# Kernel tuning notes

Measured on AMD Instinct MI355X. Metric: run time of the kernel, lower is better.

The kernel has to match this reference:

```python
import jax, jax.numpy as jnp
import numpy as np
import math

H = 1024
N = 64
DT_MIN, DT_MAX = 1e-3, 1e-1
L_SEQ = 4096


def setup_inputs() -> dict:
    key = jax.random.key(0)
    k1, k2, k3 = jax.random.split(key, 3)
    # C ~ complex normal, stored as (..., 2) real view like torch.view_as_real
    C = jax.random.normal(k1, (H, N // 2, 2), dtype=jnp.float32)
    # log_dt ~ U[log(dt_min), log(dt_max)]
    log_dt = jax.random.uniform(k2, (H,), dtype=jnp.float32) * (
        math.log(DT_MAX) - math.log(DT_MIN)
    ) + math.log(DT_MIN)
    # log_A_real = log(0.5), A_imag = pi * arange(N/2) repeated over H
    log_A_real = jnp.full((H, N // 2), math.log(0.5), dtype=jnp.float32)
    A_imag = math.pi * jnp.broadcast_to(
        jnp.arange(N // 2, dtype=jnp.float32), (H, N // 2)
    )
    return {"C": C, "log_dt": log_dt, "log_A_real": log_A_real, "A_imag": A_imag, "L": L_SEQ}


def reference(C, log_dt, log_A_real, A_imag, L):
    dt = jnp.exp(log_dt)                                  # (H,)
    Cc = jax.lax.complex(C[..., 0], C[..., 1])            # (H, N/2) complex
    A = -jnp.exp(log_A_real) + 1j * A_imag                # (H, N/2) complex
    dtA = A * dt[:, None]                                 # (H, N/2)
    # Vandermonde: exp(dtA * l) for l in [0, L)
    K = dtA[:, :, None] * jnp.arange(L, dtype=jnp.float32)  # (H, N/2, L)
    Cm = Cc * (jnp.exp(dtA) - 1.0) / A                    # (H, N/2)
    K = 2.0 * jnp.einsum("hn,hnl->hl", Cm, jnp.exp(K)).real  # (H, L)
    return K
```

## Files before the change

kernel.cpp:

```cpp
#include <hip/hip_runtime.h>
#include <hip/hip_bf16.h>
#include <math.h>


#define H_DIM 1024
#define NH 32
#define L_DIM 4096
#define TPB 256
#define PER 16
#define STRIDE_F 72

__global__ __launch_bounds__(TPB) void s4d_kernel(
    const float* __restrict__ C,
    const float* __restrict__ log_dt,
    const float* __restrict__ log_A_real,
    const float* __restrict__ A_imag,
    float* __restrict__ out)
{
    const int h = blockIdx.x;
    const int t = threadIdx.x;

    __shared__ float lds[NH * STRIDE_F];

    const double INV_2PI = 0.15915494309189533576888376337251;

    {
        const int n = t & 31;
        const int s = t >> 5;
        const float dtf = __expf(log_dt[h]);
        const float arf = -__expf(log_A_real[h * NH + n]);
        const float aif = A_imag[h * NH + n];
        const float are = arf * dtf;
        const double th_rev = (double)aif * (double)dtf * INV_2PI;

        float* base = &lds[n * STRIDE_F];

#pragma unroll
        for (int e = 0; e < 2; ++e) {
            const int j = 2 * s + e;
            {
                const int l = 16 * j;
                const float mag = __expf(are * (float)l);
                double u = (double)l * th_rev;
                u -= floor(u);
                const float uf = (float)u;
                base[8 + 2 * j]     = mag * __builtin_amdgcn_cosf(uf);
                base[8 + 2 * j + 1] = mag * __builtin_amdgcn_sinf(uf);
            }
            {
                const int l = 256 * j;
                const float mag = __expf(are * (float)l);
                double u = (double)l * th_rev;
                u -= floor(u);
                const float uf = (float)u;
                base[40 + 2 * j]     = mag * __builtin_amdgcn_cosf(uf);
                base[40 + 2 * j + 1] = mag * __builtin_amdgcn_sinf(uf);
            }
        }

        if (s == 0) {
            const float mag = __expf(are);
            double u = th_rev - floor(th_rev);
            const float uf = (float)u;
            const float wr = mag * __builtin_amdgcn_cosf(uf);
            const float wi = mag * __builtin_amdgcn_sinf(uf);
            const float cr = C[(h * NH + n) * 2 + 0];
            const float ci = C[(h * NH + n) * 2 + 1];
            const float er = wr - 1.0f;
            const float ei = wi;
            const float tr = cr * er - ci * ei;
            const float ti = cr * ei + ci * er;
            const float inv = 2.0f / (arf * arf + aif * aif);
            base[0] = wr;
            base[1] = wi;
            base[2] = (tr * arf + ti * aif) * inv;
            base[3] = (ti * arf - tr * aif) * inv;
            base[4] = wr + wr;
            base[5] = -(wr * wr + wi * wi);
        }
    }
    __syncthreads();

    float acc[PER];
#pragma unroll
    for (int j = 0; j < PER; ++j) acc[j] = 0.0f;

    const int ta_i = t & 15;
    const int tb_i = t >> 4;

#pragma unroll 2
    for (int n = 0; n < NH; ++n) {
        const float* base = &lds[n * STRIDE_F];
        const float4 hdr = *(const float4*)base;
        const float2 pq  = *(const float2*)(base + 4);
        const float2 ta  = *(const float2*)(base + 8 + 2 * ta_i);
        const float2 tb  = *(const float2*)(base + 40 + 2 * tb_i);

        const float pr = ta.x * tb.x - ta.y * tb.y;
        const float pi = ta.x * tb.y + ta.y * tb.x;
        const float zr = hdr.z * pr - hdr.w * pi;
        const float zi = hdr.z * pi + hdr.w * pr;

        float x0 = zr;
        float x1 = zr * hdr.x - zi * hdr.y;
        acc[0] += x0;
        acc[1] += x1;
        float tq = pq.y * x0;
#pragma unroll
        for (int j = 2; j < PER; ++j) {
            const float x2 = fmaf(pq.x, x1, tq);
            tq = pq.y * x1;
            acc[j] += x2;
            x0 = x1;
            x1 = x2;
        }
    }

    float4* op = (float4*)(out + (size_t)h * L_DIM + (size_t)t * PER);
#pragma unroll
    for (int j = 0; j < PER / 4; ++j) {
        op[j] = make_float4(acc[4 * j], acc[4 * j + 1], acc[4 * j + 2], acc[4 * j + 3]);
    }
}

extern "C" void kernel_launch(void* const* d_in, const int* in_sizes, int n_in,
                              void* d_out, int out_size, void* d_ws, size_t ws_size,
                              hipStream_t stream) {
    const float* C          = (const float*)d_in[0];
    const float* log_dt     = (const float*)d_in[1];
    const float* log_A_real = (const float*)d_in[2];
    const float* A_imag     = (const float*)d_in[3];
    float* out = (float*)d_out;

    s4d_kernel<<<dim3(H_DIM), dim3(TPB), 0, stream>>>(C, log_dt, log_A_real, A_imag, out);
}
```

Before: 79.16 us.

## Split sequence across two blocks per head and fold Cm into base table

Launches two blocks per head, each covering half of L, so each thread now runs an 8-step recurrence instead of 16. The fine-grained table (32 entries at stride 8) is premultiplied by Cm and the block offset, which removes a complex multiply from the inner loop. The launch bounds now request higher occupancy. The cost is that the per-block table setup (transcendentals in double-precision range reduction) runs twice as often across the grid, and the shorter recurrence gives a different accuracy profile.

```diff
diff --git a/kernel.cpp b/kernel.cpp
--- a/kernel.cpp
+++ b/kernel.cpp
@@ -6,19 +6,24 @@
 #define H_DIM 1024
 #define NH 32
 #define L_DIM 4096
+#define SPLIT 2
+#define L_BLK (L_DIM / SPLIT)
 #define TPB 256
-#define PER 16
-#define STRIDE_F 72
+#define PER 8
+#define NTA 32
+#define NTB 8
+#define STRIDE_F 84
 
-__global__ __launch_bounds__(TPB) void s4d_kernel(
+__global__ __launch_bounds__(TPB, 8) void s4d_kernel(
     const float* __restrict__ C,
     const float* __restrict__ log_dt,
     const float* __restrict__ log_A_real,
     const float* __restrict__ A_imag,
     float* __restrict__ out)
 {
-    const int h = blockIdx.x;
-    const int t = threadIdx.x;
+    const int h   = blockIdx.x;
+    const int off = blockIdx.y * L_BLK;
+    const int t   = threadIdx.x;
 
     __shared__ float lds[NH * STRIDE_F];
 
@@ -27,56 +32,57 @@
     {
         const int n = t & 31;
         const int s = t >> 5;
+
         const float dtf = __expf(log_dt[h]);
         const float arf = -__expf(log_A_real[h * NH + n]);
         const float aif = A_imag[h * NH + n];
         const float are = arf * dtf;
         const double th_rev = (double)aif * (double)dtf * INV_2PI;
 
+        const float mw = __expf(are);
+        const float u1 = (float)(th_rev - floor(th_rev));
+        const float wr = mw * __builtin_amdgcn_cosf(u1);
+        const float wi = mw * __builtin_amdgcn_sinf(u1);
+
+        const float cr = C[(h * NH + n) * 2 + 0];
+        const float ci = C[(h * NH + n) * 2 + 1];
+        const float er = wr - 1.0f;
+        const float ei = wi;
+        const float tr = cr * er - ci * ei;
+        const float ti = cr * ei + ci * er;
+        const float inv = 2.0f / (arf * arf + aif * aif);
+        const float cmr = (tr * arf + ti * aif) * inv;
+        const float cmi = (ti * arf - tr * aif) * inv;
+
         float* base = &lds[n * STRIDE_F];
 
 #pragma unroll
-        for (int e = 0; e < 2; ++e) {
-            const int j = 2 * s + e;
-            {
-                const int l = 16 * j;
-                const float mag = __expf(are * (float)l);
-                double u = (double)l * th_rev;
-                u -= floor(u);
-                const float uf = (float)u;
-                base[8 + 2 * j]     = mag * __builtin_amdgcn_cosf(uf);
-                base[8 + 2 * j + 1] = mag * __builtin_amdgcn_sinf(uf);
-            }
-            {
-                const int l = 256 * j;
-                const float mag = __expf(are * (float)l);
-                double u = (double)l * th_rev;
-                u -= floor(u);
-                const float uf = (float)u;
-                base[40 + 2 * j]     = mag * __builtin_amdgcn_cosf(uf);
-                base[40 + 2 * j + 1] = mag * __builtin_amdgcn_sinf(uf);
-            }
+        for (int k = 0; k < 4; ++k) {
+            const int i = s + 8 * k;
+            const int l = off + 8 * i;
+            const float mag = __expf(are * (float)l);
+            double u = (double)l * th_rev;
+            u -= floor(u);
+            const float uf = (float)u;
+            const float br = mag * __builtin_amdgcn_cosf(uf);
+            const float bi = mag * __builtin_amdgcn_sinf(uf);
+            base[4 + 2 * i]     = cmr * br - cmi * bi;
+            base[4 + 2 * i + 1] = cmr * bi + cmi * br;
         }
-
+        {
+            const int l = 256 * s;
+            const float mag = __expf(are * (float)l);
+            double u = (double)l * th_rev;
+            u -= floor(u);
+            const float uf = (float)u;
+            base[68 + 2 * s]     = mag * __builtin_amdgcn_cosf(uf);
+            base[68 + 2 * s + 1] = mag * __builtin_amdgcn_sinf(uf);
+        }
         if (s == 0) {
-            const float mag = __expf(are);
-            double u = th_rev - floor(th_rev);
-            const float uf = (float)u;
-            const float wr = mag * __builtin_amdgcn_cosf(uf);
-            const float wi = mag * __builtin_amdgcn_sinf(uf);
-            const float cr = C[(h * NH + n) * 2 + 0];
-            const float ci = C[(h * NH + n) * 2 + 1];
-            const float er = wr - 1.0f;
-            const float ei = wi;
-            const float tr = cr * er - ci * ei;
-            const float ti = cr * ei + ci * er;
-            const float inv = 2.0f / (arf * arf + aif * aif);
             base[0] = wr;
             base[1] = wi;
-            base[2] = (tr * arf + ti * aif) * inv;
-            base[3] = (ti * arf - tr * aif) * inv;
-            base[4] = wr + wr;
-            base[5] = -(wr * wr + wi * wi);
+            base[2] = wr + wr;
+            base[3] = -__expf(are + are);
         }
     }
     __syncthreads();
@@ -85,38 +91,35 @@
 #pragma unroll
     for (int j = 0; j < PER; ++j) acc[j] = 0.0f;
 
-    const int ta_i = t & 15;
-    const int tb_i = t >> 4;
+    const int ia = t & 31;
+    const int ib = t >> 5;
 
-#pragma unroll 2
+#pragma unroll 4
     for (int n = 0; n < NH; ++n) {
         const float* base = &lds[n * STRIDE_F];
         const float4 hdr = *(const float4*)base;
-        const float2 pq  = *(const float2*)(base + 4);
-        const float2 ta  = *(const float2*)(base + 8 + 2 * ta_i);
-        const float2 tb  = *(const float2*)(base + 40 + 2 * tb_i);
+        const float2 ta  = *(const float2*)(base + 4 + 2 * ia);
+        const float2 tb  = *(const float2*)(base + 68 + 2 * ib);
 
-        const float pr = ta.x * tb.x - ta.y * tb.y;
-        const float pi = ta.x * tb.y + ta.y * tb.x;
-        const float zr = hdr.z * pr - hdr.w * pi;
-        const float zi = hdr.z * pi + hdr.w * pr;
+        const float zr = ta.x * tb.x - ta.y * tb.y;
+        const float zi = ta.x * tb.y + ta.y * tb.x;
 
         float x0 = zr;
         float x1 = zr * hdr.x - zi * hdr.y;
         acc[0] += x0;
         acc[1] += x1;
-        float tq = pq.y * x0;
+        float tq = hdr.w * x0;
 #pragma unroll
         for (int j = 2; j < PER; ++j) {
-            const float x2 = fmaf(pq.x, x1, tq);
-            tq = pq.y * x1;
+            const float x2 = fmaf(hdr.z, x1, tq);
+            tq = hdr.w * x1;
             acc[j] += x2;
             x0 = x1;
             x1 = x2;
         }
     }
 
-    float4* op = (float4*)(out + (size_t)h * L_DIM + (size_t)t * PER);
+    float4* op = (float4*)(out + (size_t)h * L_DIM + off + t * PER);
 #pragma unroll
     for (int j = 0; j < PER / 4; ++j) {
         op[j] = make_float4(acc[4 * j], acc[4 * j + 1], acc[4 * j + 2], acc[4 * j + 3]);
@@ -132,5 +135,5 @@
     const float* A_imag     = (const float*)d_in[3];
     float* out = (float*)d_out;
 
-    s4d_kernel<<<dim3(H_DIM), dim3(TPB), 0, stream>>>(C, log_dt, log_A_real, A_imag, out);
+    s4d_kernel<<<dim3(H_DIM, SPLIT), dim3(TPB), 0, stream>>>(C, log_dt, log_A_real, A_imag, out);
 }
```

Result: no change. 79.06 us (-0.1%).
